# Kernel tuning notes

Hardware: AMD Instinct MI355X
Metric: run time of the kernel (lower is better)

Reference implementation:

```python
import jax, jax.numpy as jnp
import numpy as np

B, N, C, L = 32, 1024, 1024, 16  # batch, pixels (HW), channels, visual tokens


def setup_inputs() -> dict:
    key = jax.random.key(0)
    ks = jax.random.split(key, 18)
    s = lambda fan_in: 1.0 / np.sqrt(fan_in)
    def lin(kw, kb, fin, fout):
        W = jax.random.uniform(kw, (fin, fout), jnp.float32, -s(fin), s(fin))
        b = jax.random.uniform(kb, (fout,), jnp.float32, -s(fin), s(fin))
        return W, b
    tok_W, tok_b = lin(ks[0], ks[1], C, L)          # tokenizer pointwise conv
    key_W, key_b = lin(ks[2], ks[3], C, C // 2)     # transformer key proj
    query_W, query_b = lin(ks[4], ks[5], C, C // 2) # transformer query proj
    f1_W, f1_b = lin(ks[6], ks[7], C, C)            # FFN 1
    f2_W, f2_b = lin(ks[8], ks[9], C, C)            # FFN 2
    q_W, q_b = lin(ks[10], ks[11], C, C)            # projector W_q
    k_W, k_b = lin(ks[12], ks[13], C, C)            # projector W_k
    feature_map = jax.random.normal(ks[14], (B, N, C), jnp.float32)
    T_in = jnp.zeros((B, L, C), jnp.float32)  # unused by FilterBasedTokenizer
    return dict(feature_map=feature_map, T_in=T_in,
                tok_W=tok_W, tok_b=tok_b, key_W=key_W, key_b=key_b,
                query_W=query_W, query_b=query_b, f1_W=f1_W, f1_b=f1_b,
                f2_W=f2_W, f2_b=f2_b, q_W=q_W, q_b=q_b, k_W=k_W, k_b=k_b)


def reference(feature_map, T_in, tok_W, tok_b, key_W, key_b, query_W, query_b,
              f1_W, f1_b, f2_W, f2_b, q_W, q_b, k_W, k_b):
    X = feature_map  # [B, N, C]
    # --- FilterBasedTokenizer: softmax over pixel dim, aggregate pixels -> tokens
    proj = X @ tok_W + tok_b                         # [B, N, L]
    attn = jax.nn.softmax(proj, axis=1)              # softmax over N (dim=1)
    T = jnp.einsum('bnl,bnc->blc', attn, X)          # [B, L, C]
    # --- Transformer block on visual tokens
    k = T @ key_W + key_b                            # [B, L, C/2]
    q = T @ query_W + query_b                        # [B, L, C/2]
    scores = jnp.einsum('bld,bmd->blm', k, q)        # [B, L, L]
    T_dash = T + jax.nn.softmax(scores, axis=2) @ T  # self-attn residual
    T_out = T_dash + (jax.nn.relu(T_dash @ f1_W + f1_b) @ f2_W + f2_b)
    # --- Projector: pixels attend to tokens
    sim = jnp.einsum('bnc,blc->bnl', X @ q_W + q_b, T_out @ k_W + k_b)  # [B, N, L]
    X_out = X + jax.nn.softmax(sim, axis=2) @ T_out  # [B, N, C]
    return (X_out, T_out)
```

## Files before the change

kernel.cpp:

```cpp
#include <hip/hip_runtime.h>
#include <hip/hip_bf16.h>
#include <stdint.h>

#define BB 32
#define NN 1024
#define CC 1024
#define LL 16

typedef __attribute__((ext_vector_type(4))) float f32x4;
typedef __attribute__((ext_vector_type(8))) short short8;
typedef __attribute__((ext_vector_type(4))) unsigned short ushort4v;

__device__ __forceinline__ unsigned short f2bf(float f) {
  union { float f; unsigned u; } v; v.f = f;
  unsigned r = v.u + 0x7FFF + ((v.u >> 16) & 1);
  return (unsigned short)(r >> 16);
}
__device__ __forceinline__ float bf2f(unsigned short h) {
  union { unsigned u; float f; } v; v.u = ((unsigned)h) << 16; return v.f;
}

__global__ __launch_bounds__(256) void wprep(
    const float* __restrict__ keyW, const float* __restrict__ queryW,
    const float* __restrict__ f1W, const float* __restrict__ f2W,
    const float* __restrict__ kW, const float* __restrict__ qW,
    const float* __restrict__ tokW, const float* __restrict__ keyb,
    const float* __restrict__ queryb,
    unsigned short* __restrict__ WkqT, unsigned short* __restrict__ f1WT,
    unsigned short* __restrict__ f2WT, unsigned short* __restrict__ kWT,
    unsigned short* __restrict__ qWbf, unsigned short* __restrict__ tokWT,
    float* __restrict__ biaskq)
{
  int z = blockIdx.z;
  int tx = threadIdx.x, ty = threadIdx.y;
  if (z == 5) {
    int gid = (blockIdx.y * 32 + blockIdx.x) * 256 + ty * 32 + tx;
    if (gid < 16384) {
      int l = gid >> 10, c = gid & 1023;
      tokWT[gid] = f2bf(tokW[c * 16 + l]);
    } else if (gid < 17408) {
      int i = gid - 16384;
      biaskq[i] = (i < 512) ? keyb[i] : queryb[i - 512];
    }
    return;
  }
  if (z == 4) {
#pragma unroll
    for (int i = 0; i < 4; ++i) {
      int row = blockIdx.y * 32 + ty + 8 * i;
      int col = blockIdx.x * 32 + tx;
      qWbf[row * 1024 + col] = f2bf(qW[row * 1024 + col]);
    }
    return;
  }
  __shared__ float tile[32][33];
  int j0 = blockIdx.x * 32, k0 = blockIdx.y * 32;
  const float* src = (z == 1) ? f1W : (z == 2) ? f2W : kW;
#pragma unroll
  for (int i = 0; i < 4; ++i) {
    int k = k0 + ty + 8 * i;
    int j = j0 + tx;
    float v;
    if (z == 0) v = (j < 512) ? keyW[k * 512 + j] : queryW[k * 512 + (j - 512)];
    else        v = src[k * 1024 + j];
    tile[ty + 8 * i][tx] = v;
  }
  __syncthreads();
  unsigned short* dst = (z == 0) ? WkqT : (z == 1) ? f1WT : (z == 2) ? f2WT : kWT;
#pragma unroll
  for (int i = 0; i < 4; ++i) {
    int j = j0 + ty + 8 * i;
    dst[j * 1024 + k0 + tx] = f2bf(tile[tx][ty + 8 * i]);
  }
}

__global__ __launch_bounds__(256) void proj_mfma(
    const float* __restrict__ X, const unsigned short* __restrict__ Wt,
    const float* __restrict__ bias, float* __restrict__ out)
{
  __shared__ __align__(16) char sp[16384];
  int tid = threadIdx.x, wid = tid >> 6, lane = tid & 63;
  int lr = lane & 15, hi = lane >> 4;
  int pix0 = blockIdx.x * 64;
  int b = pix0 >> 10;
  int row = tid >> 2, seg = tid & 3;
  const float* xr = X + (size_t)(pix0 + row) * 1024 + seg * 32;
  const unsigned short* Wb = Wt + (size_t)lr * 1024 + hi * 8;
  int wbyte[4];
#pragma unroll
  for (int u = 0; u < 4; ++u)
    wbyte[u] = row * 256 + (((seg * 64 + u * 16) ^ ((row & 7) << 4)));
  int arow = wid * 16 + lr;
  int rbyte = arow * 256;
  int rx = (arow & 7) << 4;
  f32x4 acc = (f32x4)0.f;
  for (int k0 = 0; k0 < 1024; k0 += 128) {
    f32x4 v[8];
#pragma unroll
    for (int i = 0; i < 8; ++i) v[i] = *(const f32x4*)(xr + k0 + i * 4);
    __syncthreads();
#pragma unroll
    for (int u = 0; u < 4; ++u) {
      short8 pk;
      pk[0] = (short)f2bf(v[2*u][0]);   pk[1] = (short)f2bf(v[2*u][1]);
      pk[2] = (short)f2bf(v[2*u][2]);   pk[3] = (short)f2bf(v[2*u][3]);
      pk[4] = (short)f2bf(v[2*u+1][0]); pk[5] = (short)f2bf(v[2*u+1][1]);
      pk[6] = (short)f2bf(v[2*u+1][2]); pk[7] = (short)f2bf(v[2*u+1][3]);
      *(short8*)(sp + wbyte[u]) = pk;
    }
    __syncthreads();
#pragma unroll
    for (int kk = 0; kk < 4; ++kk) {
      short8 af = *(const short8*)(sp + rbyte + (((kk * 64 + hi * 16) ^ rx)));
      short8 bf = *(const short8*)(Wb + k0 + kk * 32);
      acc = __builtin_amdgcn_mfma_f32_16x16x32_bf16(af, bf, acc, 0, 0, 0);
    }
  }
  int pixb = pix0 + wid * 16 + hi * 4;
  float bv = bias[lr];
#pragma unroll
  for (int rr = 0; rr < 4; ++rr) {
    int pix = pixb + rr;
    out[((size_t)b * 16 + lr) * 1024 + (pix & 1023)] = acc[rr] + bv;
  }
}

__global__ __launch_bounds__(256) void softmax_n(float* __restrict__ projT) {
  float* row = projT + (size_t)blockIdx.x * NN;
  int t = threadIdx.x;
  f32x4 v = ((f32x4*)row)[t];
  float m = fmaxf(fmaxf(v[0], v[1]), fmaxf(v[2], v[3]));
#pragma unroll
  for (int msk = 32; msk >= 1; msk >>= 1) m = fmaxf(m, __shfl_xor(m, msk));
  __shared__ float redm[4], reds[4];
  if ((t & 63) == 0) redm[t >> 6] = m;
  __syncthreads();
  m = fmaxf(fmaxf(redm[0], redm[1]), fmaxf(redm[2], redm[3]));
  f32x4 e;
  e[0] = __expf(v[0] - m); e[1] = __expf(v[1] - m);
  e[2] = __expf(v[2] - m); e[3] = __expf(v[3] - m);
  float s = e[0] + e[1] + e[2] + e[3];
#pragma unroll
  for (int msk = 32; msk >= 1; msk >>= 1) s += __shfl_xor(s, msk);
  if ((t & 63) == 0) reds[t >> 6] = s;
  __syncthreads();
  s = reds[0] + reds[1] + reds[2] + reds[3];
  float inv = 1.f / s;
  e[0] *= inv; e[1] *= inv; e[2] *= inv; e[3] *= inv;
  ((f32x4*)row)[t] = e;
}

__global__ __launch_bounds__(256) void tpart_kernel(
    const float* __restrict__ X, const float* __restrict__ attnT,
    unsigned short* __restrict__ TpartBf)
{
  int b = blockIdx.y, ch = blockIdx.x;
  int n0 = ch * 128;
  __shared__ float att[128][16];
  int tid = threadIdx.x;
#pragma unroll
  for (int i = 0; i < 2; ++i) {
    int fi = tid + 256 * i;
    int l = fi >> 5, n4 = (fi & 31) << 2;
    f32x4 a = *(const f32x4*)&attnT[((size_t)b * 16 + l) * 1024 + n0 + n4];
    att[n4 + 0][l] = a[0]; att[n4 + 1][l] = a[1];
    att[n4 + 2][l] = a[2]; att[n4 + 3][l] = a[3];
  }
  __syncthreads();
  f32x4 acc[16];
#pragma unroll
  for (int l = 0; l < 16; ++l) acc[l] = (f32x4)0.f;
  const float* xp = X + ((size_t)b * 1024 + n0) * 1024 + tid * 4;
#pragma unroll 4
  for (int n = 0; n < 128; ++n) {
    f32x4 xv = *(const f32x4*)(xp + (size_t)n * 1024);
    const f32x4* ar = (const f32x4*)&att[n][0];
    f32x4 a0 = ar[0], a1 = ar[1], a2 = ar[2], a3 = ar[3];
    acc[0]  += a0[0]*xv; acc[1]  += a0[1]*xv; acc[2]  += a0[2]*xv; acc[3]  += a0[3]*xv;
    acc[4]  += a1[0]*xv; acc[5]  += a1[1]*xv; acc[6]  += a1[2]*xv; acc[7]  += a1[3]*xv;
    acc[8]  += a2[0]*xv; acc[9]  += a2[1]*xv; acc[10] += a2[2]*xv; acc[11] += a2[3]*xv;
    acc[12] += a3[0]*xv; acc[13] += a3[1]*xv; acc[14] += a3[2]*xv; acc[15] += a3[3]*xv;
  }
  unsigned short* op = TpartBf + (size_t)(b * 8 + ch) * 16 * 1024 + tid * 4;
#pragma unroll
  for (int l = 0; l < 16; ++l) {
    f32x4 s = acc[l];
    ushort4v h; h[0]=f2bf(s[0]); h[1]=f2bf(s[1]); h[2]=f2bf(s[2]); h[3]=f2bf(s[3]);
    *(ushort4v*)(op + (size_t)l * 1024) = h;
  }
}

__global__ void treduce(const unsigned short* __restrict__ TpartBf,
                        float* __restrict__ T, unsigned short* __restrict__ Tbf) {
  int f = blockIdx.x * 256 + threadIdx.x;
  int b = f >> 12, w = f & 4095;
  f32x4 s = (f32x4)0.f;
#pragma unroll
  for (int ch = 0; ch < 8; ++ch) {
    ushort4v h = ((const ushort4v*)TpartBf)[(size_t)(b * 8 + ch) * 4096 + w];
    s[0] += bf2f(h[0]); s[1] += bf2f(h[1]); s[2] += bf2f(h[2]); s[3] += bf2f(h[3]);
  }
  ((f32x4*)T)[f] = s;
  ushort4v h; h[0]=f2bf(s[0]); h[1]=f2bf(s[1]); h[2]=f2bf(s[2]); h[3]=f2bf(s[3]);
  ((ushort4v*)Tbf)[f] = h;
}

template<int RELU, int HAS_BIAS, int HAS_RES, int STORE_F32, int STORE_BF16>
__global__ __launch_bounds__(256) void gemm32x64(
    const unsigned short* __restrict__ A, const unsigned short* __restrict__ Bm,
    const float* __restrict__ bias, const float* __restrict__ res,
    float* __restrict__ outF, unsigned short* __restrict__ outB)
{
  const int K = 1024;
  __shared__ __align__(16) char sh[12288];
  char* Asp = sh;
  char* Bsp = sh + 4096;
  int tid = threadIdx.x, wid = tid >> 6, lane = tid & 63;
  int lr = lane & 15, hi = lane >> 4;
  int m0 = blockIdx.x * 32, n0 = blockIdx.y * 64;
  int arow = tid >> 3, acol = (tid & 7) * 8;
  int brow = tid >> 2, bcol = (tid & 3) * 16;
  const unsigned short* Ap = A + (size_t)(m0 + arow) * K + acol;
  const unsigned short* Bp = Bm + (size_t)(n0 + brow) * K + bcol;
  int aw  = arow * 128 + (((acol * 2) ^ ((arow & 7) << 4)));
  int bw0 = brow * 128 + (((bcol * 2) ^ ((brow & 7) << 4)));
  int bw1 = brow * 128 + ((((bcol * 2) + 16) ^ ((brow & 7) << 4)));
  short8 aR[2]; short8 bR[2][2];
  aR[0]    = *(const short8*)(Ap);
  bR[0][0] = *(const short8*)(Bp);
  bR[0][1] = *(const short8*)(Bp + 8);
  aR[1]    = *(const short8*)(Ap + 64);
  bR[1][0] = *(const short8*)(Bp + 64);
  bR[1][1] = *(const short8*)(Bp + 72);
  f32x4 acc[2];
  acc[0] = (f32x4)0.f; acc[1] = (f32x4)0.f;
  int wm = (wid >> 1) * 16, wn = (wid & 1) * 32;
  int arb = (wm + lr) * 128, arx = ((wm + lr) & 7) << 4;
  for (int s = 0; s < 16; ++s) {
    __syncthreads();
    *(short8*)(Asp + aw)  = aR[s & 1];
    *(short8*)(Bsp + bw0) = bR[s & 1][0];
    *(short8*)(Bsp + bw1) = bR[s & 1][1];
    __syncthreads();
    if (s + 2 < 16) {
      int k0 = (s + 2) * 64;
      aR[s & 1]    = *(const short8*)(Ap + k0);
      bR[s & 1][0] = *(const short8*)(Bp + k0);
      bR[s & 1][1] = *(const short8*)(Bp + k0 + 8);
    }
#pragma unroll
    for (int kk = 0; kk < 2; ++kk) {
      short8 af = *(const short8*)(Asp + arb + (((kk * 64 + hi * 16) ^ arx)));
#pragma unroll
      for (int sn = 0; sn < 2; ++sn) {
        int br = wn + sn * 16 + lr;
        short8 bf = *(const short8*)(Bsp + br * 128 + (((kk * 64 + hi * 16) ^ ((br & 7) << 4))));
        acc[sn] = __builtin_amdgcn_mfma_f32_16x16x32_bf16(af, bf, acc[sn], 0, 0, 0);
      }
    }
  }
  int row0 = m0 + wm + hi * 4;
#pragma unroll
  for (int sn = 0; sn < 2; ++sn) {
    int col = n0 + wn + sn * 16 + lr;
    float bv_ = HAS_BIAS ? bias[col] : 0.f;
#pragma unroll
    for (int rr = 0; rr < 4; ++rr) {
      float x = acc[sn][rr] + bv_;
      if (RELU) x = fmaxf(x, 0.f);
      size_t idx = (size_t)(row0 + rr) * 1024 + col;
      if (HAS_RES) x += res[idx];
      if (STORE_F32) outF[idx] = x;
      if (STORE_BF16) outB[idx] = f2bf(x);
    }
  }
}

__global__ __launch_bounds__(256) void scores_tdash(
    const float* __restrict__ kq, const float* __restrict__ T,
    float* __restrict__ Tdash, unsigned short* __restrict__ Tdbf)
{
  int cs = blockIdx.x, b = blockIdx.y;
  int c0 = cs * 128;
  __shared__ float Ts[16][128];
  int tid = threadIdx.x, lane = tid & 63;
#pragma unroll
  for (int i = 0; i < 2; ++i) {
    int fi = tid + 256 * i;
    int rrow = fi >> 5, c4 = (fi & 31) * 4;
    *(f32x4*)&Ts[rrow][c4] = *(const f32x4*)&T[((size_t)b * 16 + rrow) * 1024 + c0 + c4];
  }
  __syncthreads();
  int l = tid >> 4, m = tid & 15;
  const float* krow = kq + ((size_t)b * 16 + l) * 1024;
  const float* qrow = kq + ((size_t)b * 16 + m) * 1024 + 512;
  float s = 0.f;
#pragma unroll 8
  for (int d = 0; d < 512; d += 4) {
    f32x4 kv = *(const f32x4*)(krow + d);
    f32x4 qv = *(const f32x4*)(qrow + d);
    s += kv[0]*qv[0] + kv[1]*qv[1] + kv[2]*qv[2] + kv[3]*qv[3];
  }
  float mx = s;
  mx = fmaxf(mx, __shfl_xor(mx, 1)); mx = fmaxf(mx, __shfl_xor(mx, 2));
  mx = fmaxf(mx, __shfl_xor(mx, 4)); mx = fmaxf(mx, __shfl_xor(mx, 8));
  float e = __expf(s - mx);
  float sum = e;
  sum += __shfl_xor(sum, 1); sum += __shfl_xor(sum, 2);
  sum += __shfl_xor(sum, 4); sum += __shfl_xor(sum, 8);
  float pv = e / sum;
  float pl[16];
#pragma unroll
  for (int i = 0; i < 16; ++i) pl[i] = __shfl(pv, (lane & 48) + i);
  float* od = Tdash + ((size_t)b * 16 + l) * 1024 + c0;
  unsigned short* ob = Tdbf + ((size_t)b * 16 + l) * 1024 + c0;
#pragma unroll
  for (int h = 0; h < 2; ++h) {
    int c = m * 8 + h * 4;
    f32x4 o = *(const f32x4*)&Ts[l][c];
#pragma unroll
    for (int mm = 0; mm < 16; ++mm) {
      f32x4 tv = *(const f32x4*)&Ts[mm][c];
      o += pl[mm] * tv;
    }
    *(f32x4*)(od + c) = o;
    ushort4v hh; hh[0]=f2bf(o[0]); hh[1]=f2bf(o[1]); hh[2]=f2bf(o[2]); hh[3]=f2bf(o[3]);
    *(ushort4v*)(ob + c) = hh;
  }
}

__global__ __launch_bounds__(256) void r_kernel(
    const unsigned short* __restrict__ Tkbf, const float* __restrict__ qb,
    float* __restrict__ r)
{
  int row = blockIdx.x * 4 + (threadIdx.x >> 6);
  int lane = threadIdx.x & 63;
  const unsigned short* p = Tkbf + (size_t)row * CC;
  float s = 0.f;
#pragma unroll
  for (int h = 0; h < 2; ++h) {
    int d0 = lane * 8 + h * 512;
    short8 v = *(const short8*)&p[d0];
#pragma unroll
    for (int jj = 0; jj < 8; ++jj)
      s += bf2f((unsigned short)v[jj]) * qb[d0 + jj];
  }
#pragma unroll
  for (int msk = 32; msk >= 1; msk >>= 1) s += __shfl_xor(s, msk);
  if (lane == 0) r[row] = s;
}

__global__ __launch_bounds__(256) void sim_out_kernel(
    const float* __restrict__ X, const unsigned short* __restrict__ Gt,
    const float* __restrict__ rbias, const float* __restrict__ Tout,
    float* __restrict__ Xout)
{
  __shared__ __align__(16) char sp[16384];
  __shared__ float Ps[64][16];
  int tid = threadIdx.x, wid = tid >> 6, lane = tid & 63;
  int lr = lane & 15, hi = lane >> 4;
  int pix0 = blockIdx.x * 64 + blockIdx.y * 1024;
  int b = blockIdx.y;
  int row = tid >> 2, seg = tid & 3;
  const float* xr = X + (size_t)(pix0 + row) * 1024 + seg * 32;
  const unsigned short* Wb = Gt + (size_t)b * 16 * 1024 + (size_t)lr * 1024 + hi * 8;
  int wbyte[4];
#pragma unroll
  for (int u = 0; u < 4; ++u)
    wbyte[u] = row * 256 + (((seg * 64 + u * 16) ^ ((row & 7) << 4)));
  int arow = wid * 16 + lr;
  int rbyte = arow * 256;
  int rx = (arow & 7) << 4;
  f32x4 acc = (f32x4)0.f;
  for (int k0 = 0; k0 < 1024; k0 += 128) {
    f32x4 v[8];
#pragma unroll
    for (int i = 0; i < 8; ++i) v[i] = *(const f32x4*)(xr + k0 + i * 4);
    __syncthreads();
#pragma unroll
    for (int u = 0; u < 4; ++u) {
      short8 pk;
      pk[0] = (short)f2bf(v[2*u][0]);   pk[1] = (short)f2bf(v[2*u][1]);
      pk[2] = (short)f2bf(v[2*u][2]);   pk[3] = (short)f2bf(v[2*u][3]);
      pk[4] = (short)f2bf(v[2*u+1][0]); pk[5] = (short)f2bf(v[2*u+1][1]);
      pk[6] = (short)f2bf(v[2*u+1][2]); pk[7] = (short)f2bf(v[2*u+1][3]);
      *(short8*)(sp + wbyte[u]) = pk;
    }
    __syncthreads();
#pragma unroll
    for (int kk = 0; kk < 4; ++kk) {
      short8 af = *(const short8*)(sp + rbyte + (((kk * 64 + hi * 16) ^ rx)));
      short8 bf = *(const short8*)(Wb + k0 + kk * 32);
      acc = __builtin_amdgcn_mfma_f32_16x16x32_bf16(af, bf, acc, 0, 0, 0);
    }
  }
  float bv = rbias[b * 16 + lr];
  int prow = wid * 16 + hi * 4;
#pragma unroll
  for (int rr = 0; rr < 4; ++rr) {
    float vv = acc[rr] + bv;
    float mx = vv;
    mx = fmaxf(mx, __shfl_xor(mx, 1)); mx = fmaxf(mx, __shfl_xor(mx, 2));
    mx = fmaxf(mx, __shfl_xor(mx, 4)); mx = fmaxf(mx, __shfl_xor(mx, 8));
    float e = __expf(vv - mx);
    float ss = e;
    ss += __shfl_xor(ss, 1); ss += __shfl_xor(ss, 2);
    ss += __shfl_xor(ss, 4); ss += __shfl_xor(ss, 8);
    Ps[prow + rr][lr] = e / ss;
  }
  __syncthreads();
  int c4 = tid * 4;
  f32x4 tsr[16];
#pragma unroll
  for (int l = 0; l < 16; ++l)
    tsr[l] = *(const f32x4*)&Tout[((size_t)b * 16 + l) * 1024 + c4];
  const float* xp = X + (size_t)pix0 * 1024 + c4;
  float* op = Xout + (size_t)pix0 * 1024 + c4;
#pragma unroll 2
  for (int n = 0; n < 64; ++n) {
    f32x4 xv = *(const f32x4*)(xp + (size_t)n * 1024);
    const f32x4* pr = (const f32x4*)&Ps[n][0];
    f32x4 p0 = pr[0], p1 = pr[1], p2 = pr[2], p3 = pr[3];
    f32x4 o = xv;
    o += p0[0]*tsr[0];  o += p0[1]*tsr[1];  o += p0[2]*tsr[2];  o += p0[3]*tsr[3];
    o += p1[0]*tsr[4];  o += p1[1]*tsr[5];  o += p1[2]*tsr[6];  o += p1[3]*tsr[7];
    o += p2[0]*tsr[8];  o += p2[1]*tsr[9];  o += p2[2]*tsr[10]; o += p2[3]*tsr[11];
    o += p3[0]*tsr[12]; o += p3[1]*tsr[13]; o += p3[2]*tsr[14]; o += p3[3]*tsr[15];
    *(f32x4*)(op + (size_t)n * 1024) = o;
  }
}

extern "C" void kernel_launch(void* const* d_in, const int* in_sizes, int n_in,
                              void* d_out, int out_size, void* d_ws, size_t ws_size,
                              hipStream_t stream)
{
  const float* X      = (const float*)d_in[0];
  const float* tokW   = (const float*)d_in[2];
  const float* tokB   = (const float*)d_in[3];
  const float* keyW   = (const float*)d_in[4];
  const float* keyB   = (const float*)d_in[5];
  const float* queryW = (const float*)d_in[6];
  const float* queryB = (const float*)d_in[7];
  const float* f1W    = (const float*)d_in[8];
  const float* f1B    = (const float*)d_in[9];
  const float* f2W    = (const float*)d_in[10];
  const float* f2B    = (const float*)d_in[11];
  const float* qW     = (const float*)d_in[12];
  const float* qB     = (const float*)d_in[13];
  const float* kW     = (const float*)d_in[14];
  const float* kB     = (const float*)d_in[15];

  float* Xout = (float*)d_out;
  float* Tout = (float*)d_out + (size_t)BB * NN * CC;

  char* ws = (char*)d_ws;
  size_t off = 0;
  auto alloc_f = [&](size_t n) { float* pp = (float*)(ws + off); off += n * 4; return pp; };
  float* attn   = alloc_f(524288);
  float* Tbuf   = alloc_f(524288);
  float* kqbuf  = alloc_f(524288);
  float* Tdash  = alloc_f(524288);
  float* rbuf   = alloc_f(1024);
  float* biaskq = alloc_f(1024);
  auto alloc_h = [&](size_t n) { unsigned short* pp = (unsigned short*)(ws + off); off += n * 2; return pp; };
  unsigned short* TpartBf = alloc_h(4194304);
  unsigned short* Tbf    = alloc_h(524288);
  unsigned short* Tdbf   = alloc_h(524288);
  unsigned short* Hbf    = alloc_h(524288);
  unsigned short* Toutbf = alloc_h(524288);
  unsigned short* Tkbf   = alloc_h(524288);
  unsigned short* Gtbf   = alloc_h(524288);
  unsigned short* WkqT   = alloc_h(1048576);
  unsigned short* f1WT   = alloc_h(1048576);
  unsigned short* f2WT   = alloc_h(1048576);
  unsigned short* kWT    = alloc_h(1048576);
  unsigned short* qWbf   = alloc_h(1048576);
  unsigned short* tokWT  = alloc_h(16384);
  (void)ws_size; (void)in_sizes; (void)n_in; (void)out_size;

  wprep<<<dim3(32, 32, 6), dim3(32, 8), 0, stream>>>(keyW, queryW, f1W, f2W, kW, qW,
                                                     tokW, keyB, queryB,
                                                     WkqT, f1WT, f2WT, kWT, qWbf, tokWT, biaskq);
  proj_mfma<<<dim3(512), 256, 0, stream>>>(X, tokWT, tokB, attn);
  softmax_n<<<512, 256, 0, stream>>>(attn);
  tpart_kernel<<<dim3(8, 32), 256, 0, stream>>>(X, attn, TpartBf);
  treduce<<<512, 256, 0, stream>>>(TpartBf, Tbuf, Tbf);
  gemm32x64<0,1,0,1,0><<<dim3(16, 16), 256, 0, stream>>>(Tbf, WkqT, biaskq, nullptr, kqbuf, nullptr);
  scores_tdash<<<dim3(8, 32), 256, 0, stream>>>(kqbuf, Tbuf, Tdash, Tdbf);
  gemm32x64<1,1,0,0,1><<<dim3(16, 16), 256, 0, stream>>>(Tdbf, f1WT, f1B, nullptr, nullptr, Hbf);
  gemm32x64<0,1,1,1,1><<<dim3(16, 16), 256, 0, stream>>>(Hbf, f2WT, f2B, Tdash, Tout, Toutbf);
  gemm32x64<0,1,0,0,1><<<dim3(16, 16), 256, 0, stream>>>(Toutbf, kWT, kB, nullptr, nullptr, Tkbf);
  r_kernel<<<128, 256, 0, stream>>>(Tkbf, qB, rbuf);
  gemm32x64<0,0,0,0,1><<<dim3(16, 16), 256, 0, stream>>>(Tkbf, qWbf, nullptr, nullptr, nullptr, Gtbf);
  sim_out_kernel<<<dim3(16, 32), 256, 0, stream>>>(X, Gtbf, rbuf, Tout, Xout);
}
```

Measured before the change: 210.6 us.

## Fuse tokenizer projection, softmax and aggregation with online-softmax merge; split projector stage

Merges the tokenizer projection, softmax over pixels and token aggregation into one kernel that emits per-chunk partial sums with local max/sum. A new merge kernel rescales and combines them flash-style, replacing four kernels and the round trip of the attention matrix. The small GEMMs move to 32x32 tiles, doubling the block count, and the projector is split into a K-halved sim kernel, a separate softmax, and an output kernel with nontemporal stores. The projector split adds extra launches and a second read of X to gain parallelism.

```diff
diff --git a/kernel.cpp b/kernel.cpp
--- a/kernel.cpp
+++ b/kernel.cpp
@@ -74,18 +74,22 @@
   }
 }
 
-__global__ __launch_bounds__(256) void proj_mfma(
-    const float* __restrict__ X, const unsigned short* __restrict__ Wt,
-    const float* __restrict__ bias, float* __restrict__ out)
+__global__ __launch_bounds__(256) void tok_fused(
+    const float* __restrict__ X, const unsigned short* __restrict__ tokWT,
+    const float* __restrict__ tokB, unsigned short* __restrict__ Tp,
+    float* __restrict__ Mloc, float* __restrict__ Sloc)
 {
   __shared__ __align__(16) char sp[16384];
+  __shared__ float E[64][16];
+  __shared__ float redm[4][16];
+  __shared__ float reds[4][16];
   int tid = threadIdx.x, wid = tid >> 6, lane = tid & 63;
   int lr = lane & 15, hi = lane >> 4;
-  int pix0 = blockIdx.x * 64;
-  int b = pix0 >> 10;
+  int b = blockIdx.y, ch = blockIdx.x;
+  int pix0 = b * 1024 + ch * 64;
   int row = tid >> 2, seg = tid & 3;
   const float* xr = X + (size_t)(pix0 + row) * 1024 + seg * 32;
-  const unsigned short* Wb = Wt + (size_t)lr * 1024 + hi * 8;
+  const unsigned short* Wb = tokWT + lr * 1024 + hi * 8;
   int wbyte[4];
 #pragma unroll
   for (int u = 0; u < 4; ++u)
@@ -112,167 +116,159 @@
 #pragma unroll
     for (int kk = 0; kk < 4; ++kk) {
       short8 af = *(const short8*)(sp + rbyte + (((kk * 64 + hi * 16) ^ rx)));
-      short8 bf = *(const short8*)(Wb + k0 + kk * 32);
-      acc = __builtin_amdgcn_mfma_f32_16x16x32_bf16(af, bf, acc, 0, 0, 0);
-    }
-  }
-  int pixb = pix0 + wid * 16 + hi * 4;
-  float bv = bias[lr];
-#pragma unroll
-  for (int rr = 0; rr < 4; ++rr) {
-    int pix = pixb + rr;
-    out[((size_t)b * 16 + lr) * 1024 + (pix & 1023)] = acc[rr] + bv;
-  }
-}
-
-__global__ __launch_bounds__(256) void softmax_n(float* __restrict__ projT) {
-  float* row = projT + (size_t)blockIdx.x * NN;
-  int t = threadIdx.x;
-  f32x4 v = ((f32x4*)row)[t];
-  float m = fmaxf(fmaxf(v[0], v[1]), fmaxf(v[2], v[3]));
-#pragma unroll
-  for (int msk = 32; msk >= 1; msk >>= 1) m = fmaxf(m, __shfl_xor(m, msk));
-  __shared__ float redm[4], reds[4];
-  if ((t & 63) == 0) redm[t >> 6] = m;
+      short8 bfv = *(const short8*)(Wb + k0 + kk * 32);
+      acc = __builtin_amdgcn_mfma_f32_16x16x32_bf16(af, bfv, acc, 0, 0, 0);
+    }
+  }
+  float tb = tokB[lr];
+  float sv[4];
+#pragma unroll
+  for (int rr = 0; rr < 4; ++rr) sv[rr] = acc[rr] + tb;
+  float pm = fmaxf(fmaxf(sv[0], sv[1]), fmaxf(sv[2], sv[3]));
+  pm = fmaxf(pm, __shfl_xor(pm, 16));
+  pm = fmaxf(pm, __shfl_xor(pm, 32));
+  if (hi == 0) redm[wid][lr] = pm;
   __syncthreads();
-  m = fmaxf(fmaxf(redm[0], redm[1]), fmaxf(redm[2], redm[3]));
-  f32x4 e;
-  e[0] = __expf(v[0] - m); e[1] = __expf(v[1] - m);
-  e[2] = __expf(v[2] - m); e[3] = __expf(v[3] - m);
-  float s = e[0] + e[1] + e[2] + e[3];
-#pragma unroll
-  for (int msk = 32; msk >= 1; msk >>= 1) s += __shfl_xor(s, msk);
-  if ((t & 63) == 0) reds[t >> 6] = s;
+  float m = fmaxf(fmaxf(redm[0][lr], redm[1][lr]), fmaxf(redm[2][lr], redm[3][lr]));
+  float ev[4]; float ps = 0.f;
+#pragma unroll
+  for (int i = 0; i < 4; ++i) { ev[i] = __expf(sv[i] - m); ps += ev[i]; }
+  ps += __shfl_xor(ps, 16); ps += __shfl_xor(ps, 32);
+  if (hi == 0) reds[wid][lr] = ps;
+#pragma unroll
+  for (int rr = 0; rr < 4; ++rr)
+    E[wid * 16 + hi * 4 + rr][lr] = ev[rr];
   __syncthreads();
-  s = reds[0] + reds[1] + reds[2] + reds[3];
-  float inv = 1.f / s;
-  e[0] *= inv; e[1] *= inv; e[2] *= inv; e[3] *= inv;
-  ((f32x4*)row)[t] = e;
-}
-
-__global__ __launch_bounds__(256) void tpart_kernel(
-    const float* __restrict__ X, const float* __restrict__ attnT,
-    unsigned short* __restrict__ TpartBf)
-{
-  int b = blockIdx.y, ch = blockIdx.x;
-  int n0 = ch * 128;
-  __shared__ float att[128][16];
-  int tid = threadIdx.x;
-#pragma unroll
-  for (int i = 0; i < 2; ++i) {
-    int fi = tid + 256 * i;
-    int l = fi >> 5, n4 = (fi & 31) << 2;
-    f32x4 a = *(const f32x4*)&attnT[((size_t)b * 16 + l) * 1024 + n0 + n4];
-    att[n4 + 0][l] = a[0]; att[n4 + 1][l] = a[1];
-    att[n4 + 2][l] = a[2]; att[n4 + 3][l] = a[3];
-  }
-  __syncthreads();
-  f32x4 acc[16];
-#pragma unroll
-  for (int l = 0; l < 16; ++l) acc[l] = (f32x4)0.f;
-  const float* xp = X + ((size_t)b * 1024 + n0) * 1024 + tid * 4;
-#pragma unroll 4
-  for (int n = 0; n < 128; ++n) {
-    f32x4 xv = *(const f32x4*)(xp + (size_t)n * 1024);
-    const f32x4* ar = (const f32x4*)&att[n][0];
-    f32x4 a0 = ar[0], a1 = ar[1], a2 = ar[2], a3 = ar[3];
-    acc[0]  += a0[0]*xv; acc[1]  += a0[1]*xv; acc[2]  += a0[2]*xv; acc[3]  += a0[3]*xv;
-    acc[4]  += a1[0]*xv; acc[5]  += a1[1]*xv; acc[6]  += a1[2]*xv; acc[7]  += a1[3]*xv;
-    acc[8]  += a2[0]*xv; acc[9]  += a2[1]*xv; acc[10] += a2[2]*xv; acc[11] += a2[3]*xv;
-    acc[12] += a3[0]*xv; acc[13] += a3[1]*xv; acc[14] += a3[2]*xv; acc[15] += a3[3]*xv;
-  }
-  unsigned short* op = TpartBf + (size_t)(b * 8 + ch) * 16 * 1024 + tid * 4;
+  if (tid < 16) {
+    float sl = reds[0][tid] + reds[1][tid] + reds[2][tid] + reds[3][tid];
+    Mloc[(b * 16 + ch) * 16 + tid] = m;
+    Sloc[(b * 16 + ch) * 16 + tid] = sl;
+  }
+  f32x4 a16[16];
+#pragma unroll
+  for (int l = 0; l < 16; ++l) a16[l] = (f32x4)0.f;
+  const float* xp = X + (size_t)pix0 * 1024 + tid * 4;
+  for (int n0 = 0; n0 < 64; n0 += 8) {
+    f32x4 xv[8];
+#pragma unroll
+    for (int i = 0; i < 8; ++i) xv[i] = *(const f32x4*)(xp + (size_t)(n0 + i) * 1024);
+#pragma unroll
+    for (int i = 0; i < 8; ++i) {
+      const f32x4* ar = (const f32x4*)&E[n0 + i][0];
+      f32x4 a0 = ar[0], a1 = ar[1], a2 = ar[2], a3 = ar[3];
+      f32x4 x0 = xv[i];
+      a16[0]  += a0[0]*x0; a16[1]  += a0[1]*x0; a16[2]  += a0[2]*x0; a16[3]  += a0[3]*x0;
+      a16[4]  += a1[0]*x0; a16[5]  += a1[1]*x0; a16[6]  += a1[2]*x0; a16[7]  += a1[3]*x0;
+      a16[8]  += a2[0]*x0; a16[9]  += a2[1]*x0; a16[10] += a2[2]*x0; a16[11] += a2[3]*x0;
+      a16[12] += a3[0]*x0; a16[13] += a3[1]*x0; a16[14] += a3[2]*x0; a16[15] += a3[3]*x0;
+    }
+  }
+  unsigned short* op = Tp + ((size_t)(b * 16 + ch) * 16) * 1024 + tid * 4;
 #pragma unroll
   for (int l = 0; l < 16; ++l) {
-    f32x4 s = acc[l];
+    f32x4 s = a16[l];
     ushort4v h; h[0]=f2bf(s[0]); h[1]=f2bf(s[1]); h[2]=f2bf(s[2]); h[3]=f2bf(s[3]);
     *(ushort4v*)(op + (size_t)l * 1024) = h;
   }
 }
 
-__global__ void treduce(const unsigned short* __restrict__ TpartBf,
-                        float* __restrict__ T, unsigned short* __restrict__ Tbf) {
-  int f = blockIdx.x * 256 + threadIdx.x;
-  int b = f >> 12, w = f & 4095;
-  f32x4 s = (f32x4)0.f;
-#pragma unroll
-  for (int ch = 0; ch < 8; ++ch) {
-    ushort4v h = ((const ushort4v*)TpartBf)[(size_t)(b * 8 + ch) * 4096 + w];
-    s[0] += bf2f(h[0]); s[1] += bf2f(h[1]); s[2] += bf2f(h[2]); s[3] += bf2f(h[3]);
-  }
-  ((f32x4*)T)[f] = s;
-  ushort4v h; h[0]=f2bf(s[0]); h[1]=f2bf(s[1]); h[2]=f2bf(s[2]); h[3]=f2bf(s[3]);
-  ((ushort4v*)Tbf)[f] = h;
+__global__ __launch_bounds__(256) void tmerge(
+    const unsigned short* __restrict__ Tp, const float* __restrict__ Mloc,
+    const float* __restrict__ Sloc, float* __restrict__ T,
+    unsigned short* __restrict__ Tbf)
+{
+  int tid = threadIdx.x;
+  int g = blockIdx.x * 2 + (tid >> 7);
+  int b = g >> 4, l = g & 15;
+  int j = tid & 127;
+  float M = -1e30f;
+#pragma unroll
+  for (int ch = 0; ch < 16; ++ch) M = fmaxf(M, Mloc[(b * 16 + ch) * 16 + l]);
+  float w[16]; float denom = 0.f;
+#pragma unroll
+  for (int ch = 0; ch < 16; ++ch) {
+    w[ch] = __expf(Mloc[(b * 16 + ch) * 16 + l] - M);
+    denom += w[ch] * Sloc[(b * 16 + ch) * 16 + l];
+  }
+  float inv = 1.f / denom;
+  float o[8];
+#pragma unroll
+  for (int t = 0; t < 8; ++t) o[t] = 0.f;
+#pragma unroll
+  for (int ch = 0; ch < 16; ++ch) {
+    const unsigned short* p = Tp + ((size_t)((b * 16 + ch) * 16 + l)) * 1024 + j * 8;
+    short8 v = *(const short8*)p;
+    float wc = w[ch];
+#pragma unroll
+    for (int t = 0; t < 8; ++t) o[t] += wc * bf2f((unsigned short)v[t]);
+  }
+  f32x4 o0, o1; short8 hb;
+#pragma unroll
+  for (int t = 0; t < 4; ++t) {
+    float x0 = o[t] * inv, x1 = o[4 + t] * inv;
+    o0[t] = x0; o1[t] = x1;
+    hb[t] = (short)f2bf(x0); hb[4 + t] = (short)f2bf(x1);
+  }
+  *(f32x4*)(T + (size_t)g * 1024 + j * 8) = o0;
+  *(f32x4*)(T + (size_t)g * 1024 + j * 8 + 4) = o1;
+  *(short8*)(Tbf + (size_t)g * 1024 + j * 8) = hb;
 }
 
 template<int RELU, int HAS_BIAS, int HAS_RES, int STORE_F32, int STORE_BF16>
-__global__ __launch_bounds__(256) void gemm32x64(
+__global__ __launch_bounds__(256) void gemm32x32(
     const unsigned short* __restrict__ A, const unsigned short* __restrict__ Bm,
     const float* __restrict__ bias, const float* __restrict__ res,
     float* __restrict__ outF, unsigned short* __restrict__ outB)
 {
   const int K = 1024;
-  __shared__ __align__(16) char sh[12288];
+  __shared__ __align__(16) char sh[8192];
   char* Asp = sh;
   char* Bsp = sh + 4096;
   int tid = threadIdx.x, wid = tid >> 6, lane = tid & 63;
   int lr = lane & 15, hi = lane >> 4;
-  int m0 = blockIdx.x * 32, n0 = blockIdx.y * 64;
-  int arow = tid >> 3, acol = (tid & 7) * 8;
-  int brow = tid >> 2, bcol = (tid & 3) * 16;
-  const unsigned short* Ap = A + (size_t)(m0 + arow) * K + acol;
-  const unsigned short* Bp = Bm + (size_t)(n0 + brow) * K + bcol;
-  int aw  = arow * 128 + (((acol * 2) ^ ((arow & 7) << 4)));
-  int bw0 = brow * 128 + (((bcol * 2) ^ ((brow & 7) << 4)));
-  int bw1 = brow * 128 + ((((bcol * 2) + 16) ^ ((brow & 7) << 4)));
-  short8 aR[2]; short8 bR[2][2];
-  aR[0]    = *(const short8*)(Ap);
-  bR[0][0] = *(const short8*)(Bp);
-  bR[0][1] = *(const short8*)(Bp + 8);
-  aR[1]    = *(const short8*)(Ap + 64);
-  bR[1][0] = *(const short8*)(Bp + 64);
-  bR[1][1] = *(const short8*)(Bp + 72);
-  f32x4 acc[2];
-  acc[0] = (f32x4)0.f; acc[1] = (f32x4)0.f;
-  int wm = (wid >> 1) * 16, wn = (wid & 1) * 32;
-  int arb = (wm + lr) * 128, arx = ((wm + lr) & 7) << 4;
+  int m0 = blockIdx.x * 32, n0 = blockIdx.y * 32;
+  int srow = tid >> 3, scol = (tid & 7) * 8;
+  const unsigned short* Ap = A + (size_t)(m0 + srow) * K + scol;
+  const unsigned short* Bp = Bm + (size_t)(n0 + srow) * K + scol;
+  int sw = srow * 128 + (((scol * 2) ^ ((srow & 7) << 4)));
+  short8 aR[2], bR[2];
+  aR[0] = *(const short8*)(Ap);
+  bR[0] = *(const short8*)(Bp);
+  aR[1] = *(const short8*)(Ap + 64);
+  bR[1] = *(const short8*)(Bp + 64);
+  f32x4 acc = (f32x4)0.f;
+  int wm = (wid >> 1) * 16, wn = (wid & 1) * 16;
+  int ar = wm + lr, br = wn + lr;
+  int arb = ar * 128, arx = (ar & 7) << 4;
+  int brb = br * 128, brx = (br & 7) << 4;
   for (int s = 0; s < 16; ++s) {
     __syncthreads();
-    *(short8*)(Asp + aw)  = aR[s & 1];
-    *(short8*)(Bsp + bw0) = bR[s & 1][0];
-    *(short8*)(Bsp + bw1) = bR[s & 1][1];
+    *(short8*)(Asp + sw) = aR[s & 1];
+    *(short8*)(Bsp + sw) = bR[s & 1];
     __syncthreads();
     if (s + 2 < 16) {
       int k0 = (s + 2) * 64;
-      aR[s & 1]    = *(const short8*)(Ap + k0);
-      bR[s & 1][0] = *(const short8*)(Bp + k0);
-      bR[s & 1][1] = *(const short8*)(Bp + k0 + 8);
+      aR[s & 1] = *(const short8*)(Ap + k0);
+      bR[s & 1] = *(const short8*)(Bp + k0);
     }
 #pragma unroll
     for (int kk = 0; kk < 2; ++kk) {
       short8 af = *(const short8*)(Asp + arb + (((kk * 64 + hi * 16) ^ arx)));
-#pragma unroll
-      for (int sn = 0; sn < 2; ++sn) {
-        int br = wn + sn * 16 + lr;
-        short8 bf = *(const short8*)(Bsp + br * 128 + (((kk * 64 + hi * 16) ^ ((br & 7) << 4))));
-        acc[sn] = __builtin_amdgcn_mfma_f32_16x16x32_bf16(af, bf, acc[sn], 0, 0, 0);
-      }
+      short8 bf = *(const short8*)(Bsp + brb + (((kk * 64 + hi * 16) ^ brx)));
+      acc = __builtin_amdgcn_mfma_f32_16x16x32_bf16(af, bf, acc, 0, 0, 0);
     }
   }
   int row0 = m0 + wm + hi * 4;
-#pragma unroll
-  for (int sn = 0; sn < 2; ++sn) {
-    int col = n0 + wn + sn * 16 + lr;
-    float bv_ = HAS_BIAS ? bias[col] : 0.f;
-#pragma unroll
-    for (int rr = 0; rr < 4; ++rr) {
-      float x = acc[sn][rr] + bv_;
-      if (RELU) x = fmaxf(x, 0.f);
-      size_t idx = (size_t)(row0 + rr) * 1024 + col;
-      if (HAS_RES) x += res[idx];
-      if (STORE_F32) outF[idx] = x;
-      if (STORE_BF16) outB[idx] = f2bf(x);
-    }
+  int col = n0 + wn + lr;
+  float bv_ = HAS_BIAS ? bias[col] : 0.f;
+#pragma unroll
+  for (int rr = 0; rr < 4; ++rr) {
+    float x = acc[rr] + bv_;
+    if (RELU) x = fmaxf(x, 0.f);
+    size_t idx = (size_t)(row0 + rr) * 1024 + col;
+    if (HAS_RES) x += res[idx];
+    if (STORE_F32) outF[idx] = x;
+    if (STORE_BF16) outB[idx] = f2bf(x);
   }
 }
 
@@ -350,20 +346,18 @@
   if (lane == 0) r[row] = s;
 }
 
-__global__ __launch_bounds__(256) void sim_out_kernel(
+__global__ __launch_bounds__(256) void sim_part(
     const float* __restrict__ X, const unsigned short* __restrict__ Gt,
-    const float* __restrict__ rbias, const float* __restrict__ Tout,
-    float* __restrict__ Xout)
+    float* __restrict__ Spart)
 {
   __shared__ __align__(16) char sp[16384];
-  __shared__ float Ps[64][16];
   int tid = threadIdx.x, wid = tid >> 6, lane = tid & 63;
   int lr = lane & 15, hi = lane >> 4;
-  int pix0 = blockIdx.x * 64 + blockIdx.y * 1024;
-  int b = blockIdx.y;
+  int ch = blockIdx.x, kh = blockIdx.y, b = blockIdx.z;
+  int pix0 = b * 1024 + ch * 64;
   int row = tid >> 2, seg = tid & 3;
-  const float* xr = X + (size_t)(pix0 + row) * 1024 + seg * 32;
-  const unsigned short* Wb = Gt + (size_t)b * 16 * 1024 + (size_t)lr * 1024 + hi * 8;
+  const float* xr = X + (size_t)(pix0 + row) * 1024 + kh * 512 + seg * 32;
+  const unsigned short* Wb = Gt + (size_t)b * 16 * 1024 + (size_t)lr * 1024 + kh * 512 + hi * 8;
   int wbyte[4];
 #pragma unroll
   for (int u = 0; u < 4; ++u)
@@ -372,7 +366,7 @@
   int rbyte = arow * 256;
   int rx = (arow & 7) << 4;
   f32x4 acc = (f32x4)0.f;
-  for (int k0 = 0; k0 < 1024; k0 += 128) {
+  for (int k0 = 0; k0 < 512; k0 += 128) {
     f32x4 v[8];
 #pragma unroll
     for (int i = 0; i < 8; ++i) v[i] = *(const f32x4*)(xr + k0 + i * 4);
@@ -390,43 +384,70 @@
 #pragma unroll
     for (int kk = 0; kk < 4; ++kk) {
       short8 af = *(const short8*)(sp + rbyte + (((kk * 64 + hi * 16) ^ rx)));
-      short8 bf = *(const short8*)(Wb + k0 + kk * 32);
-      acc = __builtin_amdgcn_mfma_f32_16x16x32_bf16(af, bf, acc, 0, 0, 0);
-    }
-  }
-  float bv = rbias[b * 16 + lr];
-  int prow = wid * 16 + hi * 4;
-#pragma unroll
-  for (int rr = 0; rr < 4; ++rr) {
-    float vv = acc[rr] + bv;
-    float mx = vv;
-    mx = fmaxf(mx, __shfl_xor(mx, 1)); mx = fmaxf(mx, __shfl_xor(mx, 2));
-    mx = fmaxf(mx, __shfl_xor(mx, 4)); mx = fmaxf(mx, __shfl_xor(mx, 8));
-    float e = __expf(vv - mx);
-    float ss = e;
-    ss += __shfl_xor(ss, 1); ss += __shfl_xor(ss, 2);
-    ss += __shfl_xor(ss, 4); ss += __shfl_xor(ss, 8);
-    Ps[prow + rr][lr] = e / ss;
-  }
-  __syncthreads();
+      short8 bfv = *(const short8*)(Wb + k0 + kk * 32);
+      acc = __builtin_amdgcn_mfma_f32_16x16x32_bf16(af, bfv, acc, 0, 0, 0);
+    }
+  }
+  int pixb = pix0 + wid * 16 + hi * 4;
+#pragma unroll
+  for (int rr = 0; rr < 4; ++rr)
+    Spart[((size_t)kh * 32768 + pixb + rr) * 16 + lr] = acc[rr];
+}
+
+__global__ __launch_bounds__(256) void softmaxP(
+    const float* __restrict__ Spart, const float* __restrict__ r,
+    float* __restrict__ P)
+{
+  int tid = threadIdx.x;
+  int pix = blockIdx.x * 16 + (tid >> 4);
+  int l = tid & 15;
+  int b = pix >> 10;
+  float s = Spart[(size_t)pix * 16 + l] + Spart[((size_t)32768 + pix) * 16 + l]
+          + r[b * 16 + l];
+  float mx = s;
+  mx = fmaxf(mx, __shfl_xor(mx, 1)); mx = fmaxf(mx, __shfl_xor(mx, 2));
+  mx = fmaxf(mx, __shfl_xor(mx, 4)); mx = fmaxf(mx, __shfl_xor(mx, 8));
+  float e = __expf(s - mx);
+  float sum = e;
+  sum += __shfl_xor(sum, 1); sum += __shfl_xor(sum, 2);
+  sum += __shfl_xor(sum, 4); sum += __shfl_xor(sum, 8);
+  P[(size_t)pix * 16 + l] = e / sum;
+}
+
+__global__ __launch_bounds__(256) void out_kernel(
+    const float* __restrict__ X, const float* __restrict__ P,
+    const float* __restrict__ Tout, float* __restrict__ Xout)
+{
+  int b = blockIdx.y, ch = blockIdx.x;
+  int tid = threadIdx.x;
   int c4 = tid * 4;
+  int pb = b * 1024 + ch * 32;
   f32x4 tsr[16];
 #pragma unroll
   for (int l = 0; l < 16; ++l)
     tsr[l] = *(const f32x4*)&Tout[((size_t)b * 16 + l) * 1024 + c4];
-  const float* xp = X + (size_t)pix0 * 1024 + c4;
-  float* op = Xout + (size_t)pix0 * 1024 + c4;
-#pragma unroll 2
-  for (int n = 0; n < 64; ++n) {
-    f32x4 xv = *(const f32x4*)(xp + (size_t)n * 1024);
-    const f32x4* pr = (const f32x4*)&Ps[n][0];
-    f32x4 p0 = pr[0], p1 = pr[1], p2 = pr[2], p3 = pr[3];
-    f32x4 o = xv;
-    o += p0[0]*tsr[0];  o += p0[1]*tsr[1];  o += p0[2]*tsr[2];  o += p0[3]*tsr[3];
-    o += p1[0]*tsr[4];  o += p1[1]*tsr[5];  o += p1[2]*tsr[6];  o += p1[3]*tsr[7];
-    o += p2[0]*tsr[8];  o += p2[1]*tsr[9];  o += p2[2]*tsr[10]; o += p2[3]*tsr[11];
-    o += p3[0]*tsr[12]; o += p3[1]*tsr[13]; o += p3[2]*tsr[14]; o += p3[3]*tsr[15];
-    *(f32x4*)(op + (size_t)n * 1024) = o;
+  __shared__ float Ps[32][16];
+  if (tid < 128)
+    *(f32x4*)&Ps[tid >> 2][(tid & 3) * 4] =
+        *(const f32x4*)&P[((size_t)pb + (tid >> 2)) * 16 + (tid & 3) * 4];
+  __syncthreads();
+  const float* xp = X + (size_t)pb * 1024 + c4;
+  float* op = Xout + (size_t)pb * 1024 + c4;
+  for (int n0 = 0; n0 < 32; n0 += 8) {
+    f32x4 xv[8];
+#pragma unroll
+    for (int i = 0; i < 8; ++i) xv[i] = *(const f32x4*)(xp + (size_t)(n0 + i) * 1024);
+#pragma unroll
+    for (int i = 0; i < 8; ++i) {
+      const f32x4* pr = (const f32x4*)&Ps[n0 + i][0];
+      f32x4 p0 = pr[0], p1 = pr[1], p2 = pr[2], p3 = pr[3];
+      f32x4 o = xv[i];
+      o += p0[0]*tsr[0];  o += p0[1]*tsr[1];  o += p0[2]*tsr[2];  o += p0[3]*tsr[3];
+      o += p1[0]*tsr[4];  o += p1[1]*tsr[5];  o += p1[2]*tsr[6];  o += p1[3]*tsr[7];
+      o += p2[0]*tsr[8];  o += p2[1]*tsr[9];  o += p2[2]*tsr[10]; o += p2[3]*tsr[11];
+      o += p3[0]*tsr[12]; o += p3[1]*tsr[13]; o += p3[2]*tsr[14]; o += p3[3]*tsr[15];
+      __builtin_nontemporal_store(o, (f32x4*)(op + (size_t)(n0 + i) * 1024));
+    }
   }
 }
 
@@ -456,14 +477,17 @@
   char* ws = (char*)d_ws;
   size_t off = 0;
   auto alloc_f = [&](size_t n) { float* pp = (float*)(ws + off); off += n * 4; return pp; };
-  float* attn   = alloc_f(524288);
   float* Tbuf   = alloc_f(524288);
   float* kqbuf  = alloc_f(524288);
   float* Tdash  = alloc_f(524288);
+  float* Spart  = alloc_f(1048576);
+  float* Pbuf   = alloc_f(524288);
   float* rbuf   = alloc_f(1024);
   float* biaskq = alloc_f(1024);
+  float* Mloc   = alloc_f(8192);
+  float* Sloc   = alloc_f(8192);
   auto alloc_h = [&](size_t n) { unsigned short* pp = (unsigned short*)(ws + off); off += n * 2; return pp; };
-  unsigned short* TpartBf = alloc_h(4194304);
+  unsigned short* Tp     = alloc_h(8388608);
   unsigned short* Tbf    = alloc_h(524288);
   unsigned short* Tdbf   = alloc_h(524288);
   unsigned short* Hbf    = alloc_h(524288);
@@ -481,16 +505,16 @@
   wprep<<<dim3(32, 32, 6), dim3(32, 8), 0, stream>>>(keyW, queryW, f1W, f2W, kW, qW,
                                                      tokW, keyB, queryB,
                                                      WkqT, f1WT, f2WT, kWT, qWbf, tokWT, biaskq);
-  proj_mfma<<<dim3(512), 256, 0, stream>>>(X, tokWT, tokB, attn);
-  softmax_n<<<512, 256, 0, stream>>>(attn);
-  tpart_kernel<<<dim3(8, 32), 256, 0, stream>>>(X, attn, TpartBf);
-  treduce<<<512, 256, 0, stream>>>(TpartBf, Tbuf, Tbf);
-  gemm32x64<0,1,0,1,0><<<dim3(16, 16), 256, 0, stream>>>(Tbf, WkqT, biaskq, nullptr, kqbuf, nullptr);
+  tok_fused<<<dim3(16, 32), 256, 0, stream>>>(X, tokWT, tokB, Tp, Mloc, Sloc);
+  tmerge<<<256, 256, 0, stream>>>(Tp, Mloc, Sloc, Tbuf, Tbf);
+  gemm32x32<0,1,0,1,0><<<dim3(16, 32), 256, 0, stream>>>(Tbf, WkqT, biaskq, nullptr, kqbuf, nullptr);
   scores_tdash<<<dim3(8, 32), 256, 0, stream>>>(kqbuf, Tbuf, Tdash, Tdbf);
-  gemm32x64<1,1,0,0,1><<<dim3(16, 16), 256, 0, stream>>>(Tdbf, f1WT, f1B, nullptr, nullptr, Hbf);
-  gemm32x64<0,1,1,1,1><<<dim3(16, 16), 256, 0, stream>>>(Hbf, f2WT, f2B, Tdash, Tout, Toutbf);
-  gemm32x64<0,1,0,0,1><<<dim3(16, 16), 256, 0, stream>>>(Toutbf, kWT, kB, nullptr, nullptr, Tkbf);
+  gemm32x32<1,1,0,0,1><<<dim3(16, 32), 256, 0, stream>>>(Tdbf, f1WT, f1B, nullptr, nullptr, Hbf);
+  gemm32x32<0,1,1,1,1><<<dim3(16, 32), 256, 0, stream>>>(Hbf, f2WT, f2B, Tdash, Tout, Toutbf);
+  gemm32x32<0,1,0,0,1><<<dim3(16, 32), 256, 0, stream>>>(Toutbf, kWT, kB, nullptr, nullptr, Tkbf);
   r_kernel<<<128, 256, 0, stream>>>(Tkbf, qB, rbuf);
-  gemm32x64<0,0,0,0,1><<<dim3(16, 16), 256, 0, stream>>>(Tkbf, qWbf, nullptr, nullptr, nullptr, Gtbf);
-  sim_out_kernel<<<dim3(16, 32), 256, 0, stream>>>(X, Gtbf, rbuf, Tout, Xout);
-}
+  gemm32x32<0,0,0,0,1><<<dim3(16, 32), 256, 0, stream>>>(Tkbf, qWbf, nullptr, nullptr, nullptr, Gtbf);
+  sim_part<<<dim3(16, 2, 32), 256, 0, stream>>>(X, Gtbf, Spart);
+  softmaxP<<<2048, 256, 0, stream>>>(Spart, rbuf, Pbuf);
+  out_kernel<<<dim3(32, 32), 256, 0, stream>>>(X, Pbuf, Tout, Xout);
+}
```

Result: slower. 410.6 us (+95.0%).
